# Kernel optimization log

Hardware: AMD Instinct MI355X
Metric: run time of the kernel (lower is better)

## Reference

```python
import jax, jax.numpy as jnp
import numpy as np

B, N, F_IN, HID, HEADS = 4, 10000, 128, 64, 4
E = 160000
NEG_SLOPE = 0.2


def _glorot(key, shape):
    fan_in, fan_out = shape[0], shape[-1]
    lim = jnp.sqrt(6.0 / (fan_in + fan_out)).astype(jnp.float32)
    return jax.random.uniform(key, shape, jnp.float32, -lim, lim)


def setup_inputs() -> dict:
    key = jax.random.key(0)
    ks = jax.random.split(key, 10)
    x = jax.random.normal(ks[0], (B, N, F_IN), jnp.float32)
    edge_index = jax.random.randint(ks[1], (2, E), 0, N, dtype=jnp.int32)
    return {
        "x": x,
        "edge_index": edge_index,
        "W1": _glorot(ks[2], (F_IN, HEADS * HID)),
        "a_src1": _glorot(ks[3], (HEADS, HID)),
        "a_dst1": _glorot(ks[4], (HEADS, HID)),
        "b1": jnp.zeros((HID,), jnp.float32),
        "W2": _glorot(ks[5], (HID, HEADS * HID)),
        "a_src2": _glorot(ks[6], (HEADS, HID)),
        "a_dst2": _glorot(ks[7], (HEADS, HID)),
        "b2": jnp.zeros((HID,), jnp.float32),
    }


def gat_conv(x, src, dst, W, a_src, a_dst, b):
    # x: [N, F]; src/dst: [E'] (self-loops already appended)
    h = (x @ W).reshape(N, HEADS, HID)              # [N, H, C]
    al_src = jnp.einsum("nhc,hc->nh", h, a_src)      # [N, H]
    al_dst = jnp.einsum("nhc,hc->nh", h, a_dst)
    e = jax.nn.leaky_relu(al_src[src] + al_dst[dst], NEG_SLOPE)  # [E', H]
    # segment softmax over incoming edges per destination node
    m = jax.ops.segment_max(e, dst, num_segments=N)  # [N, H]
    e = jnp.exp(e - m[dst])
    s = jax.ops.segment_sum(e, dst, num_segments=N)
    alpha = e / (s[dst] + 1e-16)                     # [E', H]
    out = jax.ops.segment_sum(alpha[:, :, None] * h[src], dst, num_segments=N)  # [N, H, C]
    return out.mean(axis=1) + b                      # concat=False -> head mean


def reference(x, edge_index, W1, a_src1, a_dst1, b1, W2, a_src2, a_dst2, b2):
    loops = jnp.arange(N, dtype=edge_index.dtype)
    src = jnp.concatenate([edge_index[0], loops])
    dst = jnp.concatenate([edge_index[1], loops])

    conv1 = jax.vmap(lambda xi: gat_conv(xi, src, dst, W1, a_src1, a_dst1, b1))
    conv2 = jax.vmap(lambda xi: gat_conv(xi, src, dst, W2, a_src2, a_dst2, b2))

    h = conv1(x)                 # [B, N, HID]
    h = jax.nn.elu(h)
    h = conv2(h)
    return h
```

## Files before the change

kernel.cpp:

```cpp
#include <hip/hip_runtime.h>
#include <hip/hip_fp16.h>
#include <math.h>

#define N_NODES 10000
#define B_BATCH 4
#define F_IN_C 128
#define HID_C 64
#define HEADS_C 4
#define E_EDGES 160000
#define E_TOT (E_EDGES + N_NODES)
#define E_OCT 240000
#define NEG_SLOPE 0.2f

typedef _Float16 half8 __attribute__((ext_vector_type(8)));
typedef float f32x4 __attribute__((ext_vector_type(4)));


__device__ void wext_body(const float* __restrict__ W, const float* __restrict__ asrc,
                          const float* __restrict__ adst, __half* __restrict__ Wt,
                          int tid, int K) {
    int nc = tid / K, k = tid % K;
    float v;
    if (nc < 256) {
        v = W[k * 256 + nc];
    } else if (nc < 260) {
        int hd = nc - 256; v = 0.f;
        for (int c = 0; c < 64; c++) v += W[k * 256 + hd * 64 + c] * asrc[hd * 64 + c];
    } else if (nc < 264) {
        int hd = nc - 260; v = 0.f;
        for (int c = 0; c < 64; c++) v += W[k * 256 + hd * 64 + c] * adst[hd * 64 + c];
    } else {
        v = 0.f;
    }
    Wt[(size_t)nc * K + k] = __float2half(v);
}

__global__ void k_setup(const float* __restrict__ W1, const float* __restrict__ as1,
                        const float* __restrict__ ad1, const float* __restrict__ W2,
                        const float* __restrict__ as2, const float* __restrict__ ad2,
                        __half* __restrict__ Wt1, __half* __restrict__ Wt2,
                        int* __restrict__ deg) {
    int blk = blockIdx.x;
    if (blk < 136) {
        wext_body(W1, as1, ad1, Wt1, blk * 256 + threadIdx.x, F_IN_C);
    } else if (blk < 204) {
        wext_body(W2, as2, ad2, Wt2, (blk - 136) * 256 + threadIdx.x, HID_C);
    } else {
        int i = (blk - 204) * 256 + threadIdx.x;
        if (i < N_NODES) deg[i] = 1;
    }
}


__global__ void k_deg_count(const int* __restrict__ ei, int* __restrict__ deg) {
    int e = blockIdx.x * 256 + threadIdx.x;
    if (e < E_EDGES) atomicAdd(&deg[ei[E_EDGES + e]], 1);
}

__global__ void k_scan(const int* __restrict__ deg, int* __restrict__ offs, int* __restrict__ cursor) {
    __shared__ int lds[1024];
    int t = threadIdx.x;
    int local[10];
    int tot = 0;
#pragma unroll
    for (int j = 0; j < 10; j++) {
        int i = t * 10 + j;
        int v = (i < N_NODES) ? ((deg[i] + 7) & ~7) : 0;
        tot += v;
        local[j] = tot;
    }
    lds[t] = tot;
    __syncthreads();
    for (int ofs = 1; ofs < 1024; ofs <<= 1) {
        int v = (t >= ofs) ? lds[t - ofs] : 0;
        __syncthreads();
        lds[t] += v;
        __syncthreads();
    }
    int base = lds[t] - tot;
#pragma unroll
    for (int j = 0; j < 10; j++) {
        int i = t * 10 + j;
        if (i < N_NODES) {
            offs[i + 1] = base + local[j];
            cursor[i] = (j == 0) ? base : base + local[j - 1];
        }
    }
    if (t == 0) offs[0] = 0;
}

__global__ void k_scatter(const int* __restrict__ ei, int* __restrict__ cursor,
                          int* __restrict__ csr_b, int* __restrict__ csr_dst) {
    int e = blockIdx.x * 256 + threadIdx.x;
    if (e < E_TOT) {
        int s, d;
        if (e < E_EDGES) { s = ei[e]; d = ei[E_EDGES + e]; }
        else { s = d = e - E_EDGES; }
        int pos = atomicAdd(&cursor[d], 1);
        csr_b[pos] = s << 9;
        csr_dst[pos] = d;
    }
}

__global__ void k_pad(const int* __restrict__ cursor, const int* __restrict__ offs,
                      int* __restrict__ csr_b, int* __restrict__ csr_dst) {
    int tid = blockIdx.x * 256 + threadIdx.x;
    if (tid >= N_NODES * 8) return;
    int d = tid >> 3, ps = tid & 7;
    int pos = cursor[d] + ps;
    if (pos < offs[d + 1]) { csr_b[pos] = 0; csr_dst[pos] = -1; }
}


template <int K, typename XT>
__launch_bounds__(256)
__global__ void k_gemm(const XT* __restrict__ x, const __half* __restrict__ Wt,
                       __half* __restrict__ h2, float* __restrict__ alsrc, float* __restrict__ aldst) {
    int t = threadIdx.x;
    int w = t >> 6, lane = t & 63;
    int b = blockIdx.y;
    int node0 = blockIdx.x * 16;
    int col = lane & 15, kblk = lane >> 4;

    const XT* xr = x + ((size_t)b * N_NODES + node0 + col) * K + kblk * 8;

    f32x4 acc0 = {0.f, 0.f, 0.f, 0.f};
    f32x4 acc1 = {0.f, 0.f, 0.f, 0.f};
    f32x4 acc2 = {0.f, 0.f, 0.f, 0.f};
    f32x4 acc3 = {0.f, 0.f, 0.f, 0.f};
    f32x4 accal = {0.f, 0.f, 0.f, 0.f};

#pragma unroll
    for (int k0 = 0; k0 < K; k0 += 32) {
        half8 a;
        if constexpr (sizeof(XT) == 4) {
            float4 xa = *(const float4*)(xr + k0);
            float4 xc = *(const float4*)(xr + k0 + 4);
            a[0] = (_Float16)xa.x; a[1] = (_Float16)xa.y; a[2] = (_Float16)xa.z; a[3] = (_Float16)xa.w;
            a[4] = (_Float16)xc.x; a[5] = (_Float16)xc.y; a[6] = (_Float16)xc.z; a[7] = (_Float16)xc.w;
        } else {
            a = *(const half8*)(xr + k0);
        }
        const __half* wtk = Wt + kblk * 8 + k0;
        half8 b0 = *(const half8*)(wtk + (size_t)((w * 4 + 0) * 16 + col) * K);
        half8 b1 = *(const half8*)(wtk + (size_t)((w * 4 + 1) * 16 + col) * K);
        half8 b2 = *(const half8*)(wtk + (size_t)((w * 4 + 2) * 16 + col) * K);
        half8 b3 = *(const half8*)(wtk + (size_t)((w * 4 + 3) * 16 + col) * K);
        acc0 = __builtin_amdgcn_mfma_f32_16x16x32_f16(a, b0, acc0, 0, 0, 0);
        acc1 = __builtin_amdgcn_mfma_f32_16x16x32_f16(a, b1, acc1, 0, 0, 0);
        acc2 = __builtin_amdgcn_mfma_f32_16x16x32_f16(a, b2, acc2, 0, 0, 0);
        acc3 = __builtin_amdgcn_mfma_f32_16x16x32_f16(a, b3, acc3, 0, 0, 0);
        if (w == 0) {
            half8 bal = *(const half8*)(wtk + (size_t)(256 + col) * K);
            accal = __builtin_amdgcn_mfma_f32_16x16x32_f16(a, bal, accal, 0, 0, 0);
        }
    }

    {
        __half* dst = h2 + ((size_t)b * N_NODES + node0 + kblk * 4) * 256 + w * 64 + col;
#pragma unroll
        for (int r = 0; r < 4; r++) dst[(size_t)r * 256 + 0 * 16] = __float2half(acc0[r]);
#pragma unroll
        for (int r = 0; r < 4; r++) dst[(size_t)r * 256 + 1 * 16] = __float2half(acc1[r]);
#pragma unroll
        for (int r = 0; r < 4; r++) dst[(size_t)r * 256 + 2 * 16] = __float2half(acc2[r]);
#pragma unroll
        for (int r = 0; r < 4; r++) dst[(size_t)r * 256 + 3 * 16] = __float2half(acc3[r]);
    }
    if (w == 0 && col < 8) {
        int node = node0 + kblk * 4;
        size_t nb = (size_t)b * N_NODES;
        if (col < 4) {
            float* d = alsrc + (nb + node) * 4 + col;
#pragma unroll
            for (int r = 0; r < 4; r++) d[r * 4] = accal[r];
        } else {
            float* d = aldst + (nb + node) * 4 + (col - 4);
#pragma unroll
            for (int r = 0; r < 4; r++) d[r * 4] = accal[r];
        }
    }
}


__launch_bounds__(256)
__global__ void k_alpha(const float* __restrict__ alsrc, const float* __restrict__ aldst,
                        const int* __restrict__ csr_b, const int* __restrict__ csr_dst,
                        const int* __restrict__ offs, float* __restrict__ alpha) {
    int j = blockIdx.x * 256 + threadIdx.x;
    int e_act = offs[N_NODES];
    if (j >= e_act) return;
    int b = blockIdx.y;
    size_t base = (size_t)b * 4 * E_OCT + j;
    int dst = csr_dst[j];
    if (dst < 0) {
        alpha[base] = 0.f;
        alpha[base + E_OCT] = 0.f;
        alpha[base + (size_t)2 * E_OCT] = 0.f;
        alpha[base + (size_t)3 * E_OCT] = 0.f;
        return;
    }
    int src4 = csr_b[j] >> 7;
    const float* als = alsrc + (size_t)b * N_NODES * 4;
    float4 s4 = *(const float4*)(als + src4);
    float4 d4 = *(const float4*)(aldst + ((size_t)b * N_NODES + dst) * 4);
    float a;
    a = s4.x + d4.x; a = a > 0.f ? a : NEG_SLOPE * a; float e0 = __expf(a);
    a = s4.y + d4.y; a = a > 0.f ? a : NEG_SLOPE * a; float e1 = __expf(a);
    a = s4.z + d4.z; a = a > 0.f ? a : NEG_SLOPE * a; float e2 = __expf(a);
    a = s4.w + d4.w; a = a > 0.f ? a : NEG_SLOPE * a; float e3 = __expf(a);
    alpha[base] = e0;
    alpha[base + E_OCT] = e1;
    alpha[base + (size_t)2 * E_OCT] = e2;
    alpha[base + (size_t)3 * E_OCT] = e3;
}


#define QUAD_FMA16(p4, g0, g1, g2, g3)                                                    \
    {                                                                                     \
        float2 f01, f23;                                                                  \
        f01 = __half22float2(*(__half2*)&g0.x); f23 = __half22float2(*(__half2*)&g0.y);   \
        acc.x += p4.x * f01.x; acc.y += p4.x * f01.y; acc.z += p4.x * f23.x; acc.w += p4.x * f23.y; \
        f01 = __half22float2(*(__half2*)&g1.x); f23 = __half22float2(*(__half2*)&g1.y);   \
        acc.x += p4.y * f01.x; acc.y += p4.y * f01.y; acc.z += p4.y * f23.x; acc.w += p4.y * f23.y; \
        f01 = __half22float2(*(__half2*)&g2.x); f23 = __half22float2(*(__half2*)&g2.y);   \
        acc.x += p4.z * f01.x; acc.y += p4.z * f01.y; acc.z += p4.z * f23.x; acc.w += p4.z * f23.y; \
        f01 = __half22float2(*(__half2*)&g3.x); f23 = __half22float2(*(__half2*)&g3.y);   \
        acc.x += p4.w * f01.x; acc.y += p4.w * f01.y; acc.z += p4.w * f23.x; acc.w += p4.w * f23.y; \
        sacc += p4.x + p4.y + p4.z + p4.w;                                                \
    }

template <bool LAYER1>
__launch_bounds__(256)
__global__ void k_agg(const __half* __restrict__ h2, const float* __restrict__ alpha,
                      const int* __restrict__ offs, const int* __restrict__ csr_b,
                      const float* __restrict__ bias, void* __restrict__ outv) {
    int t = threadIdx.x;
    int bid = blockIdx.x;
    int xcd = bid & 7;
    int b = xcd >> 1;
    int local = (bid >> 3) * 2 + (xcd & 1);
    int wv = t >> 6, lane = t & 63;
    int hd = lane >> 4, cl = lane & 15;
    int dst = local * 4 + wv;

    const char* hcb = (const char*)(h2 + (size_t)b * N_NODES * 256);
    const float* ec = alpha + (size_t)(b * 4 + hd) * E_OCT;
    int s0 = offs[dst], s1 = offs[dst + 1];
    int laneoff = (hd << 7) | (cl << 3);

    float4 acc = make_float4(0.f, 0.f, 0.f, 0.f);
    float sacc = 0.f;
    int4 cA = *(const int4*)(csr_b + s0);
    int4 cB = *(const int4*)(csr_b + s0 + 4);
    float4 pA = *(const float4*)(ec + s0);
    float4 pB = *(const float4*)(ec + s0 + 4);
    uint2 g0 = *(const uint2*)(hcb + (unsigned)(cA.x + laneoff));
    uint2 g1 = *(const uint2*)(hcb + (unsigned)(cA.y + laneoff));
    uint2 g2 = *(const uint2*)(hcb + (unsigned)(cA.z + laneoff));
    uint2 g3 = *(const uint2*)(hcb + (unsigned)(cA.w + laneoff));
    uint2 g4 = *(const uint2*)(hcb + (unsigned)(cB.x + laneoff));
    uint2 g5 = *(const uint2*)(hcb + (unsigned)(cB.y + laneoff));
    uint2 g6 = *(const uint2*)(hcb + (unsigned)(cB.z + laneoff));
    uint2 g7 = *(const uint2*)(hcb + (unsigned)(cB.w + laneoff));
    int jn = (s0 + 8 < s1) ? s0 + 8 : s0;
    int4 cA2 = *(const int4*)(csr_b + jn);
    int4 cB2 = *(const int4*)(csr_b + jn + 4);
    float4 pA2 = *(const float4*)(ec + jn);
    float4 pB2 = *(const float4*)(ec + jn + 4);

    for (int j = s0 + 8; j < s1; j += 8) {
        uint2 m0 = *(const uint2*)(hcb + (unsigned)(cA2.x + laneoff));
        uint2 m1 = *(const uint2*)(hcb + (unsigned)(cA2.y + laneoff));
        uint2 m2 = *(const uint2*)(hcb + (unsigned)(cA2.z + laneoff));
        uint2 m3 = *(const uint2*)(hcb + (unsigned)(cA2.w + laneoff));
        uint2 m4 = *(const uint2*)(hcb + (unsigned)(cB2.x + laneoff));
        uint2 m5 = *(const uint2*)(hcb + (unsigned)(cB2.y + laneoff));
        uint2 m6 = *(const uint2*)(hcb + (unsigned)(cB2.z + laneoff));
        uint2 m7 = *(const uint2*)(hcb + (unsigned)(cB2.w + laneoff));
        int j2 = (j + 8 < s1) ? j + 8 : j;
        int4 cA3 = *(const int4*)(csr_b + j2);
        int4 cB3 = *(const int4*)(csr_b + j2 + 4);
        float4 pA3 = *(const float4*)(ec + j2);
        float4 pB3 = *(const float4*)(ec + j2 + 4);
        QUAD_FMA16(pA, g0, g1, g2, g3)
        QUAD_FMA16(pB, g4, g5, g6, g7)
        g0 = m0; g1 = m1; g2 = m2; g3 = m3;
        g4 = m4; g5 = m5; g6 = m6; g7 = m7;
        pA = pA2; pB = pB2;
        cA2 = cA3; cB2 = cB3; pA2 = pA3; pB2 = pB3;
    }
    QUAD_FMA16(pA, g0, g1, g2, g3)
    QUAD_FMA16(pB, g4, g5, g6, g7)

    float inv = 1.f / (sacc + 1e-16f);
    float4 v = make_float4(acc.x * inv, acc.y * inv, acc.z * inv, acc.w * inv);
#pragma unroll
    for (int o = 16; o < 64; o <<= 1) {
        v.x += __shfl_xor(v.x, o);
        v.y += __shfl_xor(v.y, o);
        v.z += __shfl_xor(v.z, o);
        v.w += __shfl_xor(v.w, o);
    }
    if (lane < 16) {
        float4 b4 = *(const float4*)(bias + cl * 4);
        float ox = v.x * 0.25f + b4.x;
        float oy = v.y * 0.25f + b4.y;
        float oz = v.z * 0.25f + b4.z;
        float ow = v.w * 0.25f + b4.w;
        if (LAYER1) {
            ox = ox > 0.f ? ox : expm1f(ox);
            oy = oy > 0.f ? oy : expm1f(oy);
            oz = oz > 0.f ? oz : expm1f(oz);
            ow = ow > 0.f ? ow : expm1f(ow);
            __half2 lo = __floats2half2_rn(ox, oy);
            __half2 hi = __floats2half2_rn(oz, ow);
            uint2 pk = make_uint2(*(unsigned*)&lo, *(unsigned*)&hi);
            *(uint2*)((__half*)outv + ((size_t)b * N_NODES + dst) * 64 + cl * 4) = pk;
        } else {
            *(float4*)((float*)outv + ((size_t)b * N_NODES + dst) * 64 + cl * 4) =
                make_float4(ox, oy, oz, ow);
        }
    }
}


extern "C" void kernel_launch(void* const* d_in, const int* in_sizes, int n_in,
                              void* d_out, int out_size, void* d_ws, size_t ws_size,
                              hipStream_t stream) {
    const float* x = (const float*)d_in[0];
    const int* ei = (const int*)d_in[1];
    const float* W1 = (const float*)d_in[2];
    const float* as1 = (const float*)d_in[3];
    const float* ad1 = (const float*)d_in[4];
    const float* b1 = (const float*)d_in[5];
    const float* W2 = (const float*)d_in[6];
    const float* as2 = (const float*)d_in[7];
    const float* ad2 = (const float*)d_in[8];
    const float* b2 = (const float*)d_in[9];
    float* out = (float*)d_out;

    char* p = (char*)d_ws;
    int* deg = (int*)p;            p += sizeof(int) * N_NODES;
    int* offs = (int*)p;           p += sizeof(int) * (N_NODES + 4);
    int* cursor = (int*)p;         p += sizeof(int) * N_NODES;
    int* csr_b = (int*)p;          p += sizeof(int) * E_OCT;
    int* csr_dst = (int*)p;        p += sizeof(int) * E_OCT;
    __half* Wt1 = (__half*)p;      p += sizeof(__half) * 272 * F_IN_C;
    __half* Wt2 = (__half*)p;      p += sizeof(__half) * 272 * HID_C;
    float* alsrc = (float*)p;      p += sizeof(float) * B_BATCH * N_NODES * 4;
    float* aldst = (float*)p;      p += sizeof(float) * B_BATCH * N_NODES * 4;
    __half* h2 = (__half*)p;       p += sizeof(__half) * (size_t)B_BATCH * N_NODES * 256;
    __half* x2 = (__half*)p;       p += sizeof(__half) * (size_t)B_BATCH * N_NODES * 64;
    p = (char*)(((size_t)p + 15) & ~(size_t)15);
    float* alpha = (float*)p;      p += sizeof(float) * (size_t)B_BATCH * 4 * E_OCT;

    k_setup<<<244, 256, 0, stream>>>(W1, as1, ad1, W2, as2, ad2, Wt1, Wt2, deg);

    k_deg_count<<<(E_EDGES + 255) / 256, 256, 0, stream>>>(ei, deg);
    k_scan<<<1, 1024, 0, stream>>>(deg, offs, cursor);
    k_scatter<<<(E_TOT + 255) / 256, 256, 0, stream>>>(ei, cursor, csr_b, csr_dst);
    k_pad<<<(N_NODES * 8 + 255) / 256, 256, 0, stream>>>(cursor, offs, csr_b, csr_dst);

    dim3 gGemm(N_NODES / 16, B_BATCH);
    dim3 gAlpha((E_OCT + 255) / 256, B_BATCH);
    int gAgg = B_BATCH * 2500;

    k_gemm<F_IN_C, float><<<gGemm, 256, 0, stream>>>(x, Wt1, h2, alsrc, aldst);
    k_alpha<<<gAlpha, 256, 0, stream>>>(alsrc, aldst, csr_b, csr_dst, offs, alpha);
    k_agg<true><<<gAgg, 256, 0, stream>>>(h2, alpha, offs, csr_b, b1, x2);

    k_gemm<HID_C, __half><<<gGemm, 256, 0, stream>>>(x2, Wt2, h2, alsrc, aldst);
    k_alpha<<<gAlpha, 256, 0, stream>>>(alsrc, aldst, csr_b, csr_dst, offs, alpha);
    k_agg<false><<<gAgg, 256, 0, stream>>>(h2, alpha, offs, csr_b, b2, out);
}
```

Measured before the change: 204.8 us.

## Fuse attention logits into aggregation and merge CSR build kernels

Drops the separate alpha kernels. The aggregation kernel now gathers alsrc per edge and computes leaky-relu and exp inline, so the per-edge alpha array is no longer written and read back. CSR construction is folded into fewer launches: degree counting moves into setup, the scan runs as an extra block of the first GEMM, and padding points at a sentinel node whose features are zero and whose logit is -1e30. This removes the csr_dst array and several launches, at the cost of extra gather loads and exp work inside the aggregation loop.

```diff
diff --git a/kernel.cpp b/kernel.cpp
--- a/kernel.cpp
+++ b/kernel.cpp
@@ -6,11 +6,12 @@
 #define B_BATCH 4
 #define F_IN_C 128
 #define HID_C 64
-#define HEADS_C 4
 #define E_EDGES 160000
 #define E_TOT (E_EDGES + N_NODES)
 #define E_OCT 240000
 #define NEG_SLOPE 0.2f
+#define SN (N_NODES + 8)
+#define SH (N_NODES + 8)
 
 typedef _Float16 half8 __attribute__((ext_vector_type(8)));
 typedef float f32x4 __attribute__((ext_vector_type(4)));
@@ -35,91 +36,45 @@
     Wt[(size_t)nc * K + k] = __float2half(v);
 }
 
+
 __global__ void k_setup(const float* __restrict__ W1, const float* __restrict__ as1,
                         const float* __restrict__ ad1, const float* __restrict__ W2,
                         const float* __restrict__ as2, const float* __restrict__ ad2,
                         __half* __restrict__ Wt1, __half* __restrict__ Wt2,
-                        int* __restrict__ deg) {
-    int blk = blockIdx.x;
+                        int* __restrict__ csr_b, __half* __restrict__ h2,
+                        float* __restrict__ alsrc, int* __restrict__ deg,
+                        const int* __restrict__ ei) {
+    int blk = blockIdx.x, t = threadIdx.x;
     if (blk < 136) {
-        wext_body(W1, as1, ad1, Wt1, blk * 256 + threadIdx.x, F_IN_C);
+        wext_body(W1, as1, ad1, Wt1, blk * 256 + t, F_IN_C);
     } else if (blk < 204) {
-        wext_body(W2, as2, ad2, Wt2, (blk - 136) * 256 + threadIdx.x, HID_C);
+        wext_body(W2, as2, ad2, Wt2, (blk - 136) * 256 + t, HID_C);
+    } else if (blk < 1142) {
+        int i = (blk - 204) * 256 + t;
+        if (i < E_OCT) csr_b[i] = N_NODES << 9;
+    } else if (blk == 1142) {
+        for (int i = t; i < 4 * 256; i += 256) {
+            int b = i >> 8, c = i & 255;
+            h2[((size_t)b * SH + N_NODES) * 256 + c] = __float2half(0.f);
+        }
+        if (t < 16) {
+            int b = t >> 2, q = t & 3;
+            alsrc[((size_t)b * SN + N_NODES) * 4 + q] = -1e30f;
+        }
     } else {
-        int i = (blk - 204) * 256 + threadIdx.x;
-        if (i < N_NODES) deg[i] = 1;
-    }
-}
-
-
-__global__ void k_deg_count(const int* __restrict__ ei, int* __restrict__ deg) {
-    int e = blockIdx.x * 256 + threadIdx.x;
-    if (e < E_EDGES) atomicAdd(&deg[ei[E_EDGES + e]], 1);
-}
-
-__global__ void k_scan(const int* __restrict__ deg, int* __restrict__ offs, int* __restrict__ cursor) {
-    __shared__ int lds[1024];
-    int t = threadIdx.x;
-    int local[10];
-    int tot = 0;
-#pragma unroll
-    for (int j = 0; j < 10; j++) {
-        int i = t * 10 + j;
-        int v = (i < N_NODES) ? ((deg[i] + 7) & ~7) : 0;
-        tot += v;
-        local[j] = tot;
-    }
-    lds[t] = tot;
-    __syncthreads();
-    for (int ofs = 1; ofs < 1024; ofs <<= 1) {
-        int v = (t >= ofs) ? lds[t - ofs] : 0;
-        __syncthreads();
-        lds[t] += v;
-        __syncthreads();
-    }
-    int base = lds[t] - tot;
-#pragma unroll
-    for (int j = 0; j < 10; j++) {
-        int i = t * 10 + j;
-        if (i < N_NODES) {
-            offs[i + 1] = base + local[j];
-            cursor[i] = (j == 0) ? base : base + local[j - 1];
-        }
-    }
-    if (t == 0) offs[0] = 0;
-}
-
-__global__ void k_scatter(const int* __restrict__ ei, int* __restrict__ cursor,
-                          int* __restrict__ csr_b, int* __restrict__ csr_dst) {
-    int e = blockIdx.x * 256 + threadIdx.x;
-    if (e < E_TOT) {
-        int s, d;
-        if (e < E_EDGES) { s = ei[e]; d = ei[E_EDGES + e]; }
-        else { s = d = e - E_EDGES; }
-        int pos = atomicAdd(&cursor[d], 1);
-        csr_b[pos] = s << 9;
-        csr_dst[pos] = d;
-    }
-}
-
-__global__ void k_pad(const int* __restrict__ cursor, const int* __restrict__ offs,
-                      int* __restrict__ csr_b, int* __restrict__ csr_dst) {
-    int tid = blockIdx.x * 256 + threadIdx.x;
-    if (tid >= N_NODES * 8) return;
-    int d = tid >> 3, ps = tid & 7;
-    int pos = cursor[d] + ps;
-    if (pos < offs[d + 1]) { csr_b[pos] = 0; csr_dst[pos] = -1; }
+        int e = (blk - 1143) * 256 + t;
+        if (e < E_EDGES) atomicAdd(&deg[ei[E_EDGES + e]], 1);
+    }
 }
 
 
 template <int K, typename XT>
-__launch_bounds__(256)
-__global__ void k_gemm(const XT* __restrict__ x, const __half* __restrict__ Wt,
-                       __half* __restrict__ h2, float* __restrict__ alsrc, float* __restrict__ aldst) {
+__device__ void gemm_body(const XT* __restrict__ x, const __half* __restrict__ Wt,
+                          __half* __restrict__ h2, float* __restrict__ alsrc,
+                          float* __restrict__ aldst, int b, int tile) {
     int t = threadIdx.x;
     int w = t >> 6, lane = t & 63;
-    int b = blockIdx.y;
-    int node0 = blockIdx.x * 16;
+    int node0 = tile * 16;
     int col = lane & 15, kblk = lane >> 4;
 
     const XT* xr = x + ((size_t)b * N_NODES + node0 + col) * K + kblk * 8;
@@ -157,7 +112,7 @@
     }
 
     {
-        __half* dst = h2 + ((size_t)b * N_NODES + node0 + kblk * 4) * 256 + w * 64 + col;
+        __half* dst = h2 + ((size_t)b * SH + node0 + kblk * 4) * 256 + w * 64 + col;
 #pragma unroll
         for (int r = 0; r < 4; r++) dst[(size_t)r * 256 + 0 * 16] = __float2half(acc0[r]);
 #pragma unroll
@@ -169,13 +124,12 @@
     }
     if (w == 0 && col < 8) {
         int node = node0 + kblk * 4;
-        size_t nb = (size_t)b * N_NODES;
         if (col < 4) {
-            float* d = alsrc + (nb + node) * 4 + col;
+            float* d = alsrc + ((size_t)b * SN + node) * 4 + col;
 #pragma unroll
             for (int r = 0; r < 4; r++) d[r * 4] = accal[r];
         } else {
-            float* d = aldst + (nb + node) * 4 + (col - 4);
+            float* d = aldst + ((size_t)b * SN + node) * 4 + (col - 4);
 #pragma unroll
             for (int r = 0; r < 4; r++) d[r * 4] = accal[r];
         }
@@ -183,58 +137,83 @@
 }
 
 
+__device__ void scan_body(const int* __restrict__ deg, int* __restrict__ offs,
+                          int* __restrict__ cursor) {
+    __shared__ int lds[256];
+    int t = threadIdx.x;
+    int i0 = t * 40;
+    int tot = 0;
+    for (int j = 0; j < 40; j++) {
+        int i = i0 + j;
+        if (i < N_NODES) tot += (deg[i] + 8) & ~7;
+    }
+    lds[t] = tot;
+    __syncthreads();
+    for (int ofs = 1; ofs < 256; ofs <<= 1) {
+        int v = (t >= ofs) ? lds[t - ofs] : 0;
+        __syncthreads();
+        lds[t] += v;
+        __syncthreads();
+    }
+    int run = lds[t] - tot;
+    for (int j = 0; j < 40; j++) {
+        int i = i0 + j;
+        if (i < N_NODES) {
+            cursor[i] = run;
+            run += (deg[i] + 8) & ~7;
+            offs[i + 1] = run;
+        }
+    }
+    if (t == 0) offs[0] = 0;
+}
+
+
 __launch_bounds__(256)
-__global__ void k_alpha(const float* __restrict__ alsrc, const float* __restrict__ aldst,
-                        const int* __restrict__ csr_b, const int* __restrict__ csr_dst,
-                        const int* __restrict__ offs, float* __restrict__ alpha) {
-    int j = blockIdx.x * 256 + threadIdx.x;
-    int e_act = offs[N_NODES];
-    if (j >= e_act) return;
-    int b = blockIdx.y;
-    size_t base = (size_t)b * 4 * E_OCT + j;
-    int dst = csr_dst[j];
-    if (dst < 0) {
-        alpha[base] = 0.f;
-        alpha[base + E_OCT] = 0.f;
-        alpha[base + (size_t)2 * E_OCT] = 0.f;
-        alpha[base + (size_t)3 * E_OCT] = 0.f;
-        return;
-    }
-    int src4 = csr_b[j] >> 7;
-    const float* als = alsrc + (size_t)b * N_NODES * 4;
-    float4 s4 = *(const float4*)(als + src4);
-    float4 d4 = *(const float4*)(aldst + ((size_t)b * N_NODES + dst) * 4);
-    float a;
-    a = s4.x + d4.x; a = a > 0.f ? a : NEG_SLOPE * a; float e0 = __expf(a);
-    a = s4.y + d4.y; a = a > 0.f ? a : NEG_SLOPE * a; float e1 = __expf(a);
-    a = s4.z + d4.z; a = a > 0.f ? a : NEG_SLOPE * a; float e2 = __expf(a);
-    a = s4.w + d4.w; a = a > 0.f ? a : NEG_SLOPE * a; float e3 = __expf(a);
-    alpha[base] = e0;
-    alpha[base + E_OCT] = e1;
-    alpha[base + (size_t)2 * E_OCT] = e2;
-    alpha[base + (size_t)3 * E_OCT] = e3;
-}
-
-
-#define QUAD_FMA16(p4, g0, g1, g2, g3)                                                    \
+__global__ void k_gemm1_scan(const float* __restrict__ x, const __half* __restrict__ Wt,
+                             __half* __restrict__ h2, float* __restrict__ alsrc,
+                             float* __restrict__ aldst, const int* __restrict__ deg,
+                             int* __restrict__ offs, int* __restrict__ cursor) {
+    int bid = blockIdx.x;
+    if (bid == 2500) { scan_body(deg, offs, cursor); return; }
+    gemm_body<F_IN_C, float>(x, Wt, h2, alsrc, aldst, bid / 625, bid % 625);
+}
+
+__launch_bounds__(256)
+__global__ void k_gemm2(const __half* __restrict__ x2, const __half* __restrict__ Wt,
+                        __half* __restrict__ h2, float* __restrict__ alsrc,
+                        float* __restrict__ aldst) {
+    gemm_body<HID_C, __half>(x2, Wt, h2, alsrc, aldst, blockIdx.y, blockIdx.x);
+}
+
+
+__global__ void k_scatter(const int* __restrict__ ei, int* __restrict__ cursor,
+                          int* __restrict__ csr_b) {
+    int e = blockIdx.x * 256 + threadIdx.x;
+    if (e < E_TOT) {
+        int s, d;
+        if (e < E_EDGES) { s = ei[e]; d = ei[E_EDGES + e]; }
+        else { s = d = e - E_EDGES; }
+        int pos = atomicAdd(&cursor[d], 1);
+        csr_b[pos] = s << 9;
+    }
+}
+
+
+#define EDGE_FMA(av, g)                                                                   \
     {                                                                                     \
-        float2 f01, f23;                                                                  \
-        f01 = __half22float2(*(__half2*)&g0.x); f23 = __half22float2(*(__half2*)&g0.y);   \
-        acc.x += p4.x * f01.x; acc.y += p4.x * f01.y; acc.z += p4.x * f23.x; acc.w += p4.x * f23.y; \
-        f01 = __half22float2(*(__half2*)&g1.x); f23 = __half22float2(*(__half2*)&g1.y);   \
-        acc.x += p4.y * f01.x; acc.y += p4.y * f01.y; acc.z += p4.y * f23.x; acc.w += p4.y * f23.y; \
-        f01 = __half22float2(*(__half2*)&g2.x); f23 = __half22float2(*(__half2*)&g2.y);   \
-        acc.x += p4.z * f01.x; acc.y += p4.z * f01.y; acc.z += p4.z * f23.x; acc.w += p4.z * f23.y; \
-        f01 = __half22float2(*(__half2*)&g3.x); f23 = __half22float2(*(__half2*)&g3.y);   \
-        acc.x += p4.w * f01.x; acc.y += p4.w * f01.y; acc.z += p4.w * f23.x; acc.w += p4.w * f23.y; \
-        sacc += p4.x + p4.y + p4.z + p4.w;                                                \
+        float e = av + ad_h; e = e > 0.f ? e : NEG_SLOPE * e; e = __expf(e);              \
+        float2 f01 = __half22float2(*(__half2*)&g.x);                                     \
+        float2 f23 = __half22float2(*(__half2*)&g.y);                                     \
+        acc.x += e * f01.x; acc.y += e * f01.y; acc.z += e * f23.x; acc.w += e * f23.y;   \
+        sacc += e;                                                                        \
     }
 
 template <bool LAYER1>
 __launch_bounds__(256)
-__global__ void k_agg(const __half* __restrict__ h2, const float* __restrict__ alpha,
-                      const int* __restrict__ offs, const int* __restrict__ csr_b,
-                      const float* __restrict__ bias, void* __restrict__ outv) {
+__global__ void k_agg(const __half* __restrict__ h2, const float* __restrict__ alsrc,
+                      const float* __restrict__ aldst, const int* __restrict__ offs,
+                      const int* __restrict__ csr_b, const float* __restrict__ bias,
+                      void* __restrict__ outv) {
     int t = threadIdx.x;
     int bid = blockIdx.x;
     int xcd = bid & 7;
@@ -244,8 +223,9 @@
     int hd = lane >> 4, cl = lane & 15;
     int dst = local * 4 + wv;
 
-    const char* hcb = (const char*)(h2 + (size_t)b * N_NODES * 256);
-    const float* ec = alpha + (size_t)(b * 4 + hd) * E_OCT;
+    const char* hcb = (const char*)(h2 + (size_t)b * SH * 256);
+    const float* als = alsrc + (size_t)b * SN * 4 + hd;
+    float ad_h = aldst[((size_t)b * SN + dst) * 4 + hd];
     int s0 = offs[dst], s1 = offs[dst + 1];
     int laneoff = (hd << 7) | (cl << 3);
 
@@ -253,8 +233,6 @@
     float sacc = 0.f;
     int4 cA = *(const int4*)(csr_b + s0);
     int4 cB = *(const int4*)(csr_b + s0 + 4);
-    float4 pA = *(const float4*)(ec + s0);
-    float4 pB = *(const float4*)(ec + s0 + 4);
     uint2 g0 = *(const uint2*)(hcb + (unsigned)(cA.x + laneoff));
     uint2 g1 = *(const uint2*)(hcb + (unsigned)(cA.y + laneoff));
     uint2 g2 = *(const uint2*)(hcb + (unsigned)(cA.z + laneoff));
@@ -263,11 +241,11 @@
     uint2 g5 = *(const uint2*)(hcb + (unsigned)(cB.y + laneoff));
     uint2 g6 = *(const uint2*)(hcb + (unsigned)(cB.z + laneoff));
     uint2 g7 = *(const uint2*)(hcb + (unsigned)(cB.w + laneoff));
+    float a0 = als[cA.x >> 7], a1 = als[cA.y >> 7], a2 = als[cA.z >> 7], a3 = als[cA.w >> 7];
+    float a4 = als[cB.x >> 7], a5 = als[cB.y >> 7], a6 = als[cB.z >> 7], a7 = als[cB.w >> 7];
     int jn = (s0 + 8 < s1) ? s0 + 8 : s0;
     int4 cA2 = *(const int4*)(csr_b + jn);
     int4 cB2 = *(const int4*)(csr_b + jn + 4);
-    float4 pA2 = *(const float4*)(ec + jn);
-    float4 pB2 = *(const float4*)(ec + jn + 4);
 
     for (int j = s0 + 8; j < s1; j += 8) {
         uint2 m0 = *(const uint2*)(hcb + (unsigned)(cA2.x + laneoff));
@@ -278,20 +256,19 @@
         uint2 m5 = *(const uint2*)(hcb + (unsigned)(cB2.y + laneoff));
         uint2 m6 = *(const uint2*)(hcb + (unsigned)(cB2.z + laneoff));
         uint2 m7 = *(const uint2*)(hcb + (unsigned)(cB2.w + laneoff));
+        float v0 = als[cA2.x >> 7], v1 = als[cA2.y >> 7], v2 = als[cA2.z >> 7], v3 = als[cA2.w >> 7];
+        float v4 = als[cB2.x >> 7], v5 = als[cB2.y >> 7], v6 = als[cB2.z >> 7], v7 = als[cB2.w >> 7];
         int j2 = (j + 8 < s1) ? j + 8 : j;
         int4 cA3 = *(const int4*)(csr_b + j2);
         int4 cB3 = *(const int4*)(csr_b + j2 + 4);
-        float4 pA3 = *(const float4*)(ec + j2);
-        float4 pB3 = *(const float4*)(ec + j2 + 4);
-        QUAD_FMA16(pA, g0, g1, g2, g3)
-        QUAD_FMA16(pB, g4, g5, g6, g7)
-        g0 = m0; g1 = m1; g2 = m2; g3 = m3;
-        g4 = m4; g5 = m5; g6 = m6; g7 = m7;
-        pA = pA2; pB = pB2;
-        cA2 = cA3; cB2 = cB3; pA2 = pA3; pB2 = pB3;
-    }
-    QUAD_FMA16(pA, g0, g1, g2, g3)
-    QUAD_FMA16(pB, g4, g5, g6, g7)
+        EDGE_FMA(a0, g0) EDGE_FMA(a1, g1) EDGE_FMA(a2, g2) EDGE_FMA(a3, g3)
+        EDGE_FMA(a4, g4) EDGE_FMA(a5, g5) EDGE_FMA(a6, g6) EDGE_FMA(a7, g7)
+        g0 = m0; g1 = m1; g2 = m2; g3 = m3; g4 = m4; g5 = m5; g6 = m6; g7 = m7;
+        a0 = v0; a1 = v1; a2 = v2; a3 = v3; a4 = v4; a5 = v5; a6 = v6; a7 = v7;
+        cA2 = cA3; cB2 = cB3;
+    }
+    EDGE_FMA(a0, g0) EDGE_FMA(a1, g1) EDGE_FMA(a2, g2) EDGE_FMA(a3, g3)
+    EDGE_FMA(a4, g4) EDGE_FMA(a5, g5) EDGE_FMA(a6, g6) EDGE_FMA(a7, g7)
 
     float inv = 1.f / (sacc + 1e-16f);
     float4 v = make_float4(acc.x * inv, acc.y * inv, acc.z * inv, acc.w * inv);
@@ -345,32 +322,20 @@
     int* offs = (int*)p;           p += sizeof(int) * (N_NODES + 4);
     int* cursor = (int*)p;         p += sizeof(int) * N_NODES;
     int* csr_b = (int*)p;          p += sizeof(int) * E_OCT;
-    int* csr_dst = (int*)p;        p += sizeof(int) * E_OCT;
     __half* Wt1 = (__half*)p;      p += sizeof(__half) * 272 * F_IN_C;
     __half* Wt2 = (__half*)p;      p += sizeof(__half) * 272 * HID_C;
-    float* alsrc = (float*)p;      p += sizeof(float) * B_BATCH * N_NODES * 4;
-    float* aldst = (float*)p;      p += sizeof(float) * B_BATCH * N_NODES * 4;
-    __half* h2 = (__half*)p;       p += sizeof(__half) * (size_t)B_BATCH * N_NODES * 256;
+    float* alsrc = (float*)p;      p += sizeof(float) * B_BATCH * SN * 4;
+    float* aldst = (float*)p;      p += sizeof(float) * B_BATCH * SN * 4;
+    __half* h2 = (__half*)p;       p += sizeof(__half) * (size_t)B_BATCH * SH * 256;
     __half* x2 = (__half*)p;       p += sizeof(__half) * (size_t)B_BATCH * N_NODES * 64;
-    p = (char*)(((size_t)p + 15) & ~(size_t)15);
-    float* alpha = (float*)p;      p += sizeof(float) * (size_t)B_BATCH * 4 * E_OCT;
-
-    k_setup<<<244, 256, 0, stream>>>(W1, as1, ad1, W2, as2, ad2, Wt1, Wt2, deg);
-
-    k_deg_count<<<(E_EDGES + 255) / 256, 256, 0, stream>>>(ei, deg);
-    k_scan<<<1, 1024, 0, stream>>>(deg, offs, cursor);
-    k_scatter<<<(E_TOT + 255) / 256, 256, 0, stream>>>(ei, cursor, csr_b, csr_dst);
-    k_pad<<<(N_NODES * 8 + 255) / 256, 256, 0, stream>>>(cursor, offs, csr_b, csr_dst);
-
-    dim3 gGemm(N_NODES / 16, B_BATCH);
-    dim3 gAlpha((E_OCT + 255) / 256, B_BATCH);
-    int gAgg = B_BATCH * 2500;
-
-    k_gemm<F_IN_C, float><<<gGemm, 256, 0, stream>>>(x, Wt1, h2, alsrc, aldst);
-    k_alpha<<<gAlpha, 256, 0, stream>>>(alsrc, aldst, csr_b, csr_dst, offs, alpha);
-    k_agg<true><<<gAgg, 256, 0, stream>>>(h2, alpha, offs, csr_b, b1, x2);
-
-    k_gemm<HID_C, __half><<<gGemm, 256, 0, stream>>>(x2, Wt2, h2, alsrc, aldst);
-    k_alpha<<<gAlpha, 256, 0, stream>>>(alsrc, aldst, csr_b, csr_dst, offs, alpha);
-    k_agg<false><<<gAgg, 256, 0, stream>>>(h2, alpha, offs, csr_b, b2, out);
-}
+
+    hipMemsetAsync(deg, 0, sizeof(int) * N_NODES, stream);
+
+    k_setup<<<1768, 256, 0, stream>>>(W1, as1, ad1, W2, as2, ad2, Wt1, Wt2,
+                                      csr_b, h2, alsrc, deg, ei);
+    k_gemm1_scan<<<2501, 256, 0, stream>>>(x, Wt1, h2, alsrc, aldst, deg, offs, cursor);
+    k_scatter<<<(E_TOT + 255) / 256, 256, 0, stream>>>(ei, cursor, csr_b);
+    k_agg<true><<<B_BATCH * 2500, 256, 0, stream>>>(h2, alsrc, aldst, offs, csr_b, b1, x2);
+    k_gemm2<<<dim3(625, B_BATCH), 256, 0, stream>>>(x2, Wt2, h2, alsrc, aldst);
+    k_agg<false><<<B_BATCH * 2500, 256, 0, stream>>>(h2, alsrc, aldst, offs, csr_b, b2, out);
+}
```

Result: faster. 199.7 us (-2.5%).
